# Kernel tuning notes

Hardware: AMD Instinct MI355X
Metric: run time of the kernel (lower is better)

Reference implementation:

```python
import jax, jax.numpy as jnp
import numpy as np

V, E, H, L, B, T = 32000, 512, 512, 4, 32, 64

def setup_inputs() -> dict:
    key = jax.random.key(0)
    ks = jax.random.split(key, 12)
    s = 0.04  # ~1/sqrt(H), matches torch LSTMCell uniform scale magnitude
    emb = jax.random.normal(ks[0], (V, E), jnp.float32) * s
    emb = emb.at[0].set(0.0)  # padding_idx=0
    return {
        'context': jax.random.normal(ks[1], (B, T, H), jnp.float32),
        'dec_input': jax.random.randint(ks[2], (B, T), 0, V),
        'h0': jax.random.normal(ks[3], (L, B, H), jnp.float32) * s,
        'c0': jax.random.normal(ks[4], (L, B, H), jnp.float32) * s,
        'emb': emb,
        'W_ih': jax.random.normal(ks[5], (L, 4 * H, E), jnp.float32) * s,
        'W_hh': jax.random.normal(ks[6], (L, 4 * H, H), jnp.float32) * s,
        'b_ih': jax.random.normal(ks[7], (L, 4 * H), jnp.float32) * s,
        'b_hh': jax.random.normal(ks[8], (L, 4 * H), jnp.float32) * s,
        'W_cls': jax.random.normal(ks[9], (V, H), jnp.float32) * s,
        'b_cls': jax.random.normal(ks[10], (V,), jnp.float32) * s,
    }

def _stack_lstm_scan(x, h0, c0, W_ih, W_hh, b_ih, b_hh):
    # x: [B,T,E] -> scan over time with L stacked LSTMCells + residual
    n_layers = W_ih.shape[0]

    def step(carry, x_t):
        h, c = carry  # each [L,B,H]
        inp = x_t
        new_h, new_c = [], []
        for i in range(n_layers):
            gates = inp @ W_ih[i].T + b_ih[i] + h[i] @ W_hh[i].T + b_hh[i]
            ig, fg, gg, og = jnp.split(gates, 4, axis=-1)  # torch order: i,f,g,o
            ci = jax.nn.sigmoid(fg) * c[i] + jax.nn.sigmoid(ig) * jnp.tanh(gg)
            hi = jax.nn.sigmoid(og) * jnp.tanh(ci)
            # residual when dims match (E == H here)
            inp = hi + inp if inp.shape[-1] == hi.shape[-1] else hi
            new_h.append(hi)
            new_c.append(ci)
        return (jnp.stack(new_h), jnp.stack(new_c)), inp

    (hT, cT), outs = jax.lax.scan(step, (h0, c0), jnp.swapaxes(x, 0, 1))
    return jnp.swapaxes(outs, 0, 1), hT, cT  # [B,T,H]

def reference(context, dec_input, h0, c0, emb, W_ih, W_hh, b_ih, b_hh, W_cls, b_cls):
    x = emb[dec_input]  # [B,T,E]; dropouts are identity (p=0 / eval)
    outs, hT, cT = _stack_lstm_scan(x, h0, c0, W_ih, W_hh, b_ih, b_hh)
    logits = outs @ W_cls.T + b_cls  # [B,T,V]
    # original applies log_softmax over dim=1 (the sequence dim) - faithful
    out = jax.nn.log_softmax(logits, axis=1)
    return (out, hT, cT)
```

## Files before the change

### kernel.cpp

```cpp
#include <hip/hip_runtime.h>
#include <math.h>

#define VOCAB 32000
#define HDIM  512
#define NLAYERS 4
#define BATCH 32
#define TSTEPS 64
typedef unsigned long long ULL;

typedef __attribute__((ext_vector_type(8))) short bf16x8;
typedef __attribute__((ext_vector_type(4))) float f32x4;
typedef __attribute__((ext_vector_type(4))) unsigned int u32x4;

static __device__ __forceinline__ unsigned short f2b(float f) {
    union { float f; unsigned u; } v; v.f = f;
    return (unsigned short)((v.u + 0x7FFFu + ((v.u >> 16) & 1u)) >> 16);
}
static __device__ __forceinline__ float sigf(float x) { return 1.0f / (1.0f + __expf(-x)); }

static __device__ __forceinline__ int apack_off(int m, int k) {
    int k0 = k >> 5, mi = m >> 4;
    int lane = (m & 15) | (((k >> 3) & 3) << 4);
    return ((k0 * 2 + mi) * 64 + lane) * 8 + (k & 7);
}

__global__ void k_prep_all(
    const float* __restrict__ W_ih, const float* __restrict__ W_hh,
    const float* __restrict__ b_ih, const float* __restrict__ b_hh,
    const float* __restrict__ W_cls, const float* __restrict__ emb,
    const int* __restrict__ dec, const float* __restrict__ h0,
    unsigned short* __restrict__ wp, float* __restrict__ bs,
    unsigned short* __restrict__ wpC, float* __restrict__ seqF,
    unsigned short* __restrict__ seqBp, unsigned short* __restrict__ apack,
    unsigned* __restrict__ flags) {
    int blk = blockIdx.x;
    if (blk < 4096) {
        const int total = NLAYERS * 64 * 2 * 32 * 64 * 8;
        for (int idx = blk * 256 + threadIdx.x; idx < total; idx += 4096 * 256) {
            int sub = idx & 7, lane = (idx >> 3) & 63, k0 = (idx >> 9) & 31;
            int ni = (idx >> 14) & 1, bi = (idx >> 15) & 63, l = idx >> 21;
            int r = ni * 16 + (lane & 15);
            int k = k0 * 32 + ((lane >> 4) << 3) + sub;
            int j = (r & 3) * 512 + bi * 8 + (r >> 2);
            float v = (k < 512) ? W_ih[((size_t)l * 2048 + j) * 512 + k]
                                : W_hh[((size_t)l * 2048 + j) * 512 + (k - 512)];
            wp[idx] = f2b(v);
        }
    } else if (blk < 12096) {
        int idx8 = (blk - 4096) * 256 + threadIdx.x;
        int lane = idx8 & 63, k0 = (idx8 >> 6) & 15, ni = (idx8 >> 10) & 1;
        int w = (idx8 >> 11) & 3, vt = idx8 >> 13;
        int v = vt * 128 + w * 32 + ni * 16 + (lane & 15);
        int kb = k0 * 32 + ((lane >> 4) << 3);
        const float* src = W_cls + (size_t)v * 512 + kb;
        float4 f0 = *(const float4*)(src);
        float4 f1 = *(const float4*)(src + 4);
        bf16x8 u;
        u[0] = (short)f2b(f0.x); u[1] = (short)f2b(f0.y);
        u[2] = (short)f2b(f0.z); u[3] = (short)f2b(f0.w);
        u[4] = (short)f2b(f1.x); u[5] = (short)f2b(f1.y);
        u[6] = (short)f2b(f1.z); u[7] = (short)f2b(f1.w);
        *(bf16x8*)(wpC + (size_t)idx8 * 8) = u;
    } else if (blk < 12160) {
        int t = blk - 12096;
        for (int i = threadIdx.x; i < BATCH * HDIM; i += blockDim.x) {
            int b = i >> 9, e = i & 511;
            int tok = dec[b * TSTEPS + t];
            float v = emb[(size_t)tok * HDIM + e];
            seqF[((size_t)t * BATCH + b) * HDIM + e] = v;
            seqBp[(size_t)t * 16384 + apack_off(b, e)] = f2b(v);
        }
    } else if (blk < 12416) {
        int idx = (blk - 12160) * 256 + threadIdx.x;
        int l = idx >> 14, b = (idx >> 9) & 31, d = idx & 511;
        apack[(size_t)(l * 2) * 32768 + apack_off(b, 512 + d)] =
            f2b(h0[((size_t)l * BATCH + b) * HDIM + d]);
    } else if (blk < 12448) {
        int idx = (blk - 12416) * 256 + threadIdx.x;
        if (idx < NLAYERS * 64 * 32) {
            int r = idx & 31, bi = (idx >> 5) & 63, l = idx >> 11;
            int j = (r & 3) * 512 + bi * 8 + (r >> 2);
            bs[idx] = b_ih[l * 2048 + j] + b_hh[l * 2048 + j];
        }
    } else {
        for (int i = threadIdx.x; i < 4096; i += 256) flags[i] = 0;
    }
}

__global__ __launch_bounds__(256, 1) void k_lstm(
    unsigned short* apack,
    const unsigned short* __restrict__ wpack,
    const float* __restrict__ bsum,
    const unsigned short* __restrict__ seqBp,
    const float* __restrict__ seqF,
    float* outF,
    unsigned short* __restrict__ seqOut,
    const float* __restrict__ c0,
    float* __restrict__ outHT, float* __restrict__ outCT,
    unsigned* flags) {
    const int l = blockIdx.x >> 6, bi = blockIdx.x & 63;
    const int wave = threadIdx.x >> 6, lane = threadIdx.x & 63;
    const int mi = wave >> 1, ni = wave & 1;
    const int cb = threadIdx.x >> 3, dsl = threadIdx.x & 7;
    const int d = bi * 8 + dsl;

    __shared__ __align__(16) short sW[32768];
    __shared__ __align__(16) short sA[32768];
    __shared__ __align__(16) float sG[1024];
    __shared__ __align__(16) short sHexH[512];
    __shared__ __align__(16) short sHexO[512];

    {
        const unsigned short* wp = wpack + (size_t)blockIdx.x * 32768;
        #pragma unroll
        for (int i = 0; i < 16; ++i) {
            int off = (i * 256 + threadIdx.x) * 8;
            *(bf16x8*)(sW + off) = *(const bf16x8*)(wp + off);
        }
    }
    float4 bias = *(const float4*)(bsum + blockIdx.x * 32 + dsl * 4);
    float c = c0[((size_t)l * BATCH + cb) * HDIM + d];

    unsigned short* A0 = apack + (size_t)(l * 2 + 0) * 32768;
    unsigned short* A1 = apack + (size_t)(l * 2 + 1) * 32768;

    for (int t = 0; t < TSTEPS; ++t) {
        if (l == 0) {
            const unsigned short* sp = seqBp + (size_t)t * 16384;
            #pragma unroll
            for (int i = 0; i < 8; ++i) {
                int off = (i * 256 + threadIdx.x) * 8;
                *(bf16x8*)(sA + off) = *(const bf16x8*)(sp + off);
            }
        }

        if (wave == 0 && t > 0) {
            const unsigned* fp = flags + (l * 64 + lane) * 16;
            while (__hip_atomic_load(fp, __ATOMIC_RELAXED, __HIP_MEMORY_SCOPE_AGENT)
                   < (unsigned)t)
                __builtin_amdgcn_s_sleep(1);
        }
        if (wave == 1 && l > 0) {
            const unsigned* fp = flags + ((l - 1) * 64 + lane) * 16;
            while (__hip_atomic_load(fp, __ATOMIC_RELAXED, __HIP_MEMORY_SCOPE_AGENT)
                   < (unsigned)(t + 1))
                __builtin_amdgcn_s_sleep(1);
        }
        if (wave == 2 && l < 3 && t > 0) {
            const unsigned* fp = flags + ((l + 1) * 64 + lane) * 16;
            while (__hip_atomic_load(fp, __ATOMIC_RELAXED, __HIP_MEMORY_SCOPE_AGENT)
                   < (unsigned)(t - 1))
                __builtin_amdgcn_s_sleep(1);
        }
        __syncthreads();

        float inpf;
        if (l == 0) inpf = seqF[((size_t)t * BATCH + cb) * HDIM + d];
        else inpf = __hip_atomic_load(&outF[(size_t)((l * 2 + (t & 1)) * BATCH + cb) * HDIM + d],
                                      __ATOMIC_RELAXED, __HIP_MEMORY_SCOPE_AGENT);

        const unsigned short* Ab = (t & 1) ? A1 : A0;
        const ULL* Abu = (const ULL*)Ab;
        ULL* sAu = (ULL*)sA;
        if (l == 0) {
            ULL tmp[16];
            #pragma unroll
            for (int i = 0; i < 16; ++i)
                tmp[i] = __hip_atomic_load(&Abu[(16 + i) * 256 + threadIdx.x],
                                           __ATOMIC_RELAXED, __HIP_MEMORY_SCOPE_AGENT);
            #pragma unroll
            for (int i = 0; i < 16; ++i)
                sAu[(16 + i) * 256 + threadIdx.x] = tmp[i];
        } else {
            ULL tmp[32];
            #pragma unroll
            for (int i = 0; i < 32; ++i)
                tmp[i] = __hip_atomic_load(&Abu[i * 256 + threadIdx.x],
                                           __ATOMIC_RELAXED, __HIP_MEMORY_SCOPE_AGENT);
            #pragma unroll
            for (int i = 0; i < 32; ++i)
                sAu[i * 256 + threadIdx.x] = tmp[i];
        }
        __syncthreads();

        f32x4 acc = {0.f, 0.f, 0.f, 0.f};
        const short* abase = sA + mi * 512 + lane * 8;
        const short* wbase = sW + ni * 16384 + lane * 8;
        #pragma unroll
        for (int k0 = 0; k0 < 32; ++k0)
            acc = __builtin_amdgcn_mfma_f32_16x16x32_bf16(
                *(const bf16x8*)(abase + k0 * 1024),
                *(const bf16x8*)(wbase + k0 * 512), acc, 0, 0, 0);

        int gb = mi * 16 + (lane >> 4) * 4;
        int gr = ni * 16 + (lane & 15);
        #pragma unroll
        for (int r = 0; r < 4; ++r) sG[(gb + r) * 32 + gr] = acc[r];
        __syncthreads();

        float4 g4 = *(const float4*)(sG + cb * 32 + dsl * 4);
        float gi = g4.x + bias.x, gf = g4.y + bias.y;
        float gg = g4.z + bias.z, go = g4.w + bias.w;
        float ci = sigf(gf) * c + sigf(gi) * tanhf(gg);
        float hi = sigf(go) * tanhf(ci);
        c = ci;
        float o = hi + inpf;

        sHexH[threadIdx.x] = f2b(hi);
        sHexO[threadIdx.x] = f2b(o);
        if (l < 3)
            __hip_atomic_store(&outF[(size_t)(((l + 1) * 2 + (t & 1)) * BATCH + cb) * HDIM + d],
                               o, __ATOMIC_RELAXED, __HIP_MEMORY_SCOPE_AGENT);
        if (t == TSTEPS - 1) {
            outHT[((size_t)l * BATCH + cb) * HDIM + d] = hi;
            outCT[((size_t)l * BATCH + cb) * HDIM + d] = ci;
        }
        __syncthreads();

        unsigned short* An = ((t + 1) & 1) ? A1 : A0;
        int i = threadIdx.x & 63, cbe = i >> 1, jh = i & 1;
        int lanecode = ((cbe & 15) | ((bi & 3) << 4)) * 2 + jh;
        if (threadIdx.x < 64) {
            int hoff = ((16 + (bi >> 2)) * 2 + (cbe >> 4)) * 128 + lanecode;
            __hip_atomic_store(&((ULL*)An)[hoff], ((const ULL*)sHexH)[i],
                               __ATOMIC_RELAXED, __HIP_MEMORY_SCOPE_AGENT);
        } else if (threadIdx.x < 128) {
            if (l < 3) {
                unsigned short* Anx = apack + (size_t)((l + 1) * 2 + (t & 1)) * 32768;
                int ooff = ((bi >> 2) * 2 + (cbe >> 4)) * 128 + lanecode;
                __hip_atomic_store(&((ULL*)Anx)[ooff], ((const ULL*)sHexO)[i],
                                   __ATOMIC_RELAXED, __HIP_MEMORY_SCOPE_AGENT);
            } else {
                int ulidx = ((((cbe * 16 + (bi >> 2)) * 4 + (t >> 4)) * 64 +
                             ((t & 15) | ((bi & 3) << 4))) * 2) + jh;
                ((ULL*)seqOut)[ulidx] = ((const ULL*)sHexO)[i];
            }
        }

        asm volatile("s_waitcnt vmcnt(0)" ::: "memory");
        __syncthreads();
        if (threadIdx.x == 0)
            __hip_atomic_store(&flags[(l * 64 + bi) * 16], (unsigned)(t + 1),
                               __ATOMIC_RELAXED, __HIP_MEMORY_SCOPE_AGENT);
    }
}

__global__ __launch_bounds__(256) void k_cls(
    const unsigned short* __restrict__ Ap,
    const unsigned short* __restrict__ Wp,
    float* __restrict__ out) {
    int bp = blockIdx.x & 15;
    int vt = blockIdx.x >> 4;
    int wave = threadIdx.x >> 6;
    int lane = threadIdx.x & 63;

    __shared__ float sL[64 * 132];

    const unsigned short* abase = Ap + (size_t)(bp * 2) * 32768 + lane * 8;
    const unsigned short* wbase = Wp + (size_t)(vt * 4 + wave) * 16384 + lane * 8;

    f32x4 acc[2][4][2];
    #pragma unroll
    for (int s = 0; s < 2; ++s)
        #pragma unroll
        for (int i = 0; i < 4; ++i)
            #pragma unroll
            for (int j = 0; j < 2; ++j) acc[s][i][j] = (f32x4)(0.0f);

    for (int k0 = 0; k0 < 16; ++k0) {
        bf16x8 bb[2];
        #pragma unroll
        for (int ni = 0; ni < 2; ++ni)
            bb[ni] = *(const bf16x8*)(wbase + ni * 8192 + k0 * 512);
        #pragma unroll
        for (int s = 0; s < 2; ++s) {
            bf16x8 a[4];
            #pragma unroll
            for (int mi = 0; mi < 4; ++mi)
                a[mi] = *(const bf16x8*)(abase + s * 32768 + (k0 * 4 + mi) * 512);
            #pragma unroll
            for (int mi = 0; mi < 4; ++mi)
                #pragma unroll
                for (int ni = 0; ni < 2; ++ni)
                    acc[s][mi][ni] = __builtin_amdgcn_mfma_f32_16x16x32_bf16(
                        a[mi], bb[ni], acc[s][mi][ni], 0, 0, 0);
        }
    }

    #pragma unroll
    for (int s = 0; s < 2; ++s) {
        if (s) __syncthreads();
        #pragma unroll
        for (int ni = 0; ni < 2; ++ni) {
            float m = -1e30f;
            #pragma unroll
            for (int mi = 0; mi < 4; ++mi)
                #pragma unroll
                for (int r = 0; r < 4; ++r) m = fmaxf(m, acc[s][mi][ni][r]);
            m = fmaxf(m, __shfl_xor(m, 16));
            m = fmaxf(m, __shfl_xor(m, 32));
            float sum = 0.f;
            #pragma unroll
            for (int mi = 0; mi < 4; ++mi)
                #pragma unroll
                for (int r = 0; r < 4; ++r) sum += expf(acc[s][mi][ni][r] - m);
            sum += __shfl_xor(sum, 16);
            sum += __shfl_xor(sum, 32);
            float logZ = m + logf(sum);
            int col = wave * 32 + ni * 16 + (lane & 15);
            #pragma unroll
            for (int mi = 0; mi < 4; ++mi) {
                #pragma unroll
                for (int r = 0; r < 4; ++r) {
                    int row = mi * 16 + (lane >> 4) * 4 + r;
                    sL[row * 132 + col] = acc[s][mi][ni][r] - logZ;
                }
            }
        }
        __syncthreads();

        float* obase = out + (size_t)(bp * 2 + s) * TSTEPS * VOCAB + vt * 128;
        #pragma unroll
        for (int it = 0; it < 8; ++it) {
            int idx = it * 256 + threadIdx.x;
            int row = idx >> 5, c4 = (idx & 31) * 4;
            f32x4 val = *(const f32x4*)(sL + row * 132 + c4);
            __builtin_nontemporal_store(val, (f32x4*)(obase + (size_t)row * VOCAB + c4));
        }
    }
}

extern "C" void kernel_launch(void* const* d_in, const int* in_sizes, int n_in,
                              void* d_out, int out_size, void* d_ws, size_t ws_size,
                              hipStream_t stream) {
    const int*   dec   = (const int*)d_in[1];
    const float* h0    = (const float*)d_in[2];
    const float* c0    = (const float*)d_in[3];
    const float* emb   = (const float*)d_in[4];
    const float* W_ih  = (const float*)d_in[5];
    const float* W_hh  = (const float*)d_in[6];
    const float* b_ih  = (const float*)d_in[7];
    const float* b_hh  = (const float*)d_in[8];
    const float* W_cls = (const float*)d_in[9];

    const int LBH = NLAYERS * BATCH * HDIM;
    const size_t BTV = (size_t)BATCH * TSTEPS * VOCAB;

    char* ws = (char*)d_ws;
    size_t off = 0;
    auto alloc = [&](size_t bytes) -> void* {
        void* p = ws + off;
        off = (off + bytes + 255) & ~(size_t)255;
        return p;
    };
    unsigned short* wpack  = (unsigned short*)alloc((size_t)NLAYERS * 64 * 2 * 32 * 64 * 8 * 2);
    float*          bsum   = (float*)alloc((size_t)NLAYERS * 64 * 32 * 4);
    unsigned short* wpackC = (unsigned short*)alloc((size_t)VOCAB * HDIM * 2);
    float*          seqF   = (float*)alloc((size_t)TSTEPS * BATCH * HDIM * 4);
    unsigned short* seqBp  = (unsigned short*)alloc((size_t)TSTEPS * 16384 * 2);
    unsigned short* apack  = (unsigned short*)alloc((size_t)NLAYERS * 2 * 32768 * 2);
    float*          outF   = (float*)alloc((size_t)NLAYERS * 2 * BATCH * HDIM * 4);
    unsigned short* apackC = (unsigned short*)alloc((size_t)TSTEPS * BATCH * HDIM * 2);
    unsigned*       flags  = (unsigned*)alloc(16384);

    k_prep_all<<<12449, 256, 0, stream>>>(W_ih, W_hh, b_ih, b_hh, W_cls, emb, dec, h0,
                                          wpack, bsum, wpackC, seqF, seqBp, apack, flags);

    k_lstm<<<256, 256, 0, stream>>>(apack, wpack, bsum, seqBp, seqF, outF, apackC,
                                    c0,
                                    (float*)d_out + BTV,
                                    (float*)d_out + BTV + LBH,
                                    flags);

    k_cls<<<250 * 16, 256, 0, stream>>>(apackC, wpackC, (float*)d_out);
}
```

Before: 458.4 us.

## Pack LSTM weights directly into LDS in k_lstm and swizzle classifier block order

```diff
diff --git a/kernel.cpp b/kernel.cpp
--- a/kernel.cpp
+++ b/kernel.cpp
@@ -10,7 +10,6 @@
 
 typedef __attribute__((ext_vector_type(8))) short bf16x8;
 typedef __attribute__((ext_vector_type(4))) float f32x4;
-typedef __attribute__((ext_vector_type(4))) unsigned int u32x4;
 
 static __device__ __forceinline__ unsigned short f2b(float f) {
     union { float f; unsigned u; } v; v.f = f;
@@ -25,29 +24,16 @@
 }
 
 __global__ void k_prep_all(
-    const float* __restrict__ W_ih, const float* __restrict__ W_hh,
     const float* __restrict__ b_ih, const float* __restrict__ b_hh,
     const float* __restrict__ W_cls, const float* __restrict__ emb,
     const int* __restrict__ dec, const float* __restrict__ h0,
-    unsigned short* __restrict__ wp, float* __restrict__ bs,
+    float* __restrict__ bs,
     unsigned short* __restrict__ wpC, float* __restrict__ seqF,
     unsigned short* __restrict__ seqBp, unsigned short* __restrict__ apack,
     unsigned* __restrict__ flags) {
     int blk = blockIdx.x;
-    if (blk < 4096) {
-        const int total = NLAYERS * 64 * 2 * 32 * 64 * 8;
-        for (int idx = blk * 256 + threadIdx.x; idx < total; idx += 4096 * 256) {
-            int sub = idx & 7, lane = (idx >> 3) & 63, k0 = (idx >> 9) & 31;
-            int ni = (idx >> 14) & 1, bi = (idx >> 15) & 63, l = idx >> 21;
-            int r = ni * 16 + (lane & 15);
-            int k = k0 * 32 + ((lane >> 4) << 3) + sub;
-            int j = (r & 3) * 512 + bi * 8 + (r >> 2);
-            float v = (k < 512) ? W_ih[((size_t)l * 2048 + j) * 512 + k]
-                                : W_hh[((size_t)l * 2048 + j) * 512 + (k - 512)];
-            wp[idx] = f2b(v);
-        }
-    } else if (blk < 12096) {
-        int idx8 = (blk - 4096) * 256 + threadIdx.x;
+    if (blk < 8000) {
+        int idx8 = blk * 256 + threadIdx.x;
         int lane = idx8 & 63, k0 = (idx8 >> 6) & 15, ni = (idx8 >> 10) & 1;
         int w = (idx8 >> 11) & 3, vt = idx8 >> 13;
         int v = vt * 128 + w * 32 + ni * 16 + (lane & 15);
@@ -61,8 +47,8 @@
         u[4] = (short)f2b(f1.x); u[5] = (short)f2b(f1.y);
         u[6] = (short)f2b(f1.z); u[7] = (short)f2b(f1.w);
         *(bf16x8*)(wpC + (size_t)idx8 * 8) = u;
-    } else if (blk < 12160) {
-        int t = blk - 12096;
+    } else if (blk < 8064) {
+        int t = blk - 8000;
         for (int i = threadIdx.x; i < BATCH * HDIM; i += blockDim.x) {
             int b = i >> 9, e = i & 511;
             int tok = dec[b * TSTEPS + t];
@@ -70,13 +56,13 @@
             seqF[((size_t)t * BATCH + b) * HDIM + e] = v;
             seqBp[(size_t)t * 16384 + apack_off(b, e)] = f2b(v);
         }
-    } else if (blk < 12416) {
-        int idx = (blk - 12160) * 256 + threadIdx.x;
+    } else if (blk < 8320) {
+        int idx = (blk - 8064) * 256 + threadIdx.x;
         int l = idx >> 14, b = (idx >> 9) & 31, d = idx & 511;
         apack[(size_t)(l * 2) * 32768 + apack_off(b, 512 + d)] =
             f2b(h0[((size_t)l * BATCH + b) * HDIM + d]);
-    } else if (blk < 12448) {
-        int idx = (blk - 12416) * 256 + threadIdx.x;
+    } else if (blk < 8352) {
+        int idx = (blk - 8320) * 256 + threadIdx.x;
         if (idx < NLAYERS * 64 * 32) {
             int r = idx & 31, bi = (idx >> 5) & 63, l = idx >> 11;
             int j = (r & 3) * 512 + bi * 8 + (r >> 2);
@@ -89,7 +75,8 @@
 
 __global__ __launch_bounds__(256, 1) void k_lstm(
     unsigned short* apack,
-    const unsigned short* __restrict__ wpack,
+    const float* __restrict__ W_ih,
+    const float* __restrict__ W_hh,
     const float* __restrict__ bsum,
     const unsigned short* __restrict__ seqBp,
     const float* __restrict__ seqF,
@@ -111,11 +98,17 @@
     __shared__ __align__(16) short sHexO[512];
 
     {
-        const unsigned short* wp = wpack + (size_t)blockIdx.x * 32768;
-        #pragma unroll
-        for (int i = 0; i < 16; ++i) {
-            int off = (i * 256 + threadIdx.x) * 8;
-            *(bf16x8*)(sW + off) = *(const bf16x8*)(wp + off);
+        #pragma unroll 4
+        for (int ii = 0; ii < 128; ++ii) {
+            int idx = ii * 256 + threadIdx.x;
+            int sub = idx & 7, lane2 = (idx >> 3) & 63, k0 = (idx >> 9) & 31;
+            int ni2 = idx >> 14;
+            int r = ni2 * 16 + (lane2 & 15);
+            int k = k0 * 32 + ((lane2 >> 4) << 3) + sub;
+            int j = (r & 3) * 512 + bi * 8 + (r >> 2);
+            float v = (k < 512) ? W_ih[((size_t)l * 2048 + j) * 512 + k]
+                                : W_hh[((size_t)l * 2048 + j) * 512 + (k - 512)];
+            sW[idx] = (short)f2b(v);
         }
     }
     float4 bias = *(const float4*)(bsum + blockIdx.x * 32 + dsl * 4);
@@ -249,8 +242,10 @@
     const unsigned short* __restrict__ Ap,
     const unsigned short* __restrict__ Wp,
     float* __restrict__ out) {
-    int bp = blockIdx.x & 15;
-    int vt = blockIdx.x >> 4;
+    int bid = blockIdx.x;
+    int u = (bid & 7) * 500 + (bid >> 3);
+    int bp = u & 15;
+    int vt = u >> 4;
     int wave = threadIdx.x >> 6;
     int lane = threadIdx.x & 63;
 
@@ -353,7 +348,6 @@
         off = (off + bytes + 255) & ~(size_t)255;
         return p;
     };
-    unsigned short* wpack  = (unsigned short*)alloc((size_t)NLAYERS * 64 * 2 * 32 * 64 * 8 * 2);
     float*          bsum   = (float*)alloc((size_t)NLAYERS * 64 * 32 * 4);
     unsigned short* wpackC = (unsigned short*)alloc((size_t)VOCAB * HDIM * 2);
     float*          seqF   = (float*)alloc((size_t)TSTEPS * BATCH * HDIM * 4);
@@ -363,10 +357,10 @@
     unsigned short* apackC = (unsigned short*)alloc((size_t)TSTEPS * BATCH * HDIM * 2);
     unsigned*       flags  = (unsigned*)alloc(16384);
 
-    k_prep_all<<<12449, 256, 0, stream>>>(W_ih, W_hh, b_ih, b_hh, W_cls, emb, dec, h0,
-                                          wpack, bsum, wpackC, seqF, seqBp, apack, flags);
-
-    k_lstm<<<256, 256, 0, stream>>>(apack, wpack, bsum, seqBp, seqF, outF, apackC,
+    k_prep_all<<<8353, 256, 0, stream>>>(b_ih, b_hh, W_cls, emb, dec, h0,
+                                         bsum, wpackC, seqF, seqBp, apack, flags);
+
+    k_lstm<<<256, 256, 0, stream>>>(apack, W_ih, W_hh, bsum, seqBp, seqF, outF, apackC,
                                     c0,
                                     (float*)d_out + BTV,
                                     (float*)d_out + BTV + LBH,
```

Measured after the change: 437.3 us. 4.6% less time.
